# Kernel tuning notes

Hardware: AMD Instinct MI355X
Metric: run time of the kernel (lower is better)

The kernel has to match this reference:

```python
import jax, jax.numpy as jnp
import numpy as np

N = 100000
E = 1600000


def _sage(x, src, dst, wl, wr, b):
    # PyG SAGEConv: out = lin_l(mean_{j in N(i)} x_j) + lin_r(x_i)
    agg = jax.ops.segment_sum(x[src], dst, num_segments=N)
    cnt = jax.ops.segment_sum(jnp.ones((src.shape[0], 1), x.dtype), dst, num_segments=N)
    mean = agg / jnp.maximum(cnt, 1.0)
    return mean @ wl.T + x @ wr.T + b


def _tag(x, src, dst, norm, K, w, b):
    # PyG TAGConv: concat of K+1 hops of D^-1/2 A D^-1/2 propagation, one Linear
    xs = [x]
    h = x
    for _ in range(K):
        h = jax.ops.segment_sum(h[src] * norm[:, None], dst, num_segments=N)
        xs.append(h)
    return jnp.concatenate(xs, axis=1) @ w.T + b


def setup_inputs() -> dict:
    key = jax.random.key(0)
    ks = iter(jax.random.split(key, 32))
    x = jax.random.normal(next(ks), (N, 11), dtype=jnp.float32)
    edge_index = jax.random.randint(next(ks), (2, E), 0, N, dtype=jnp.int64)

    def w(k, o, i):
        return jax.random.normal(k, (o, i), dtype=jnp.float32) / np.sqrt(i)

    p = {
        'sage1_wl': w(next(ks), 128, 11), 'sage1_wr': w(next(ks), 128, 11), 'sage1_b': jnp.zeros((128,), jnp.float32),
        'sage2_wl': w(next(ks), 128, 128), 'sage2_wr': w(next(ks), 128, 128), 'sage2_b': jnp.zeros((128,), jnp.float32),
        'sage3_wl': w(next(ks), 1, 128), 'sage3_wr': w(next(ks), 1, 128), 'sage3_b': jnp.zeros((1,), jnp.float32),
        'tag1a_w': w(next(ks), 8, 44), 'tag1a_b': jnp.zeros((8,), jnp.float32),
        'tag2a_w': w(next(ks), 1, 32), 'tag2a_b': jnp.zeros((1,), jnp.float32),
        'tag1b_w': w(next(ks), 8, 77), 'tag1b_b': jnp.zeros((8,), jnp.float32),
        'tag2b_w': w(next(ks), 1, 56), 'tag2b_b': jnp.zeros((1,), jnp.float32),
        'lin1_w': w(next(ks), 1, 3), 'lin1_b': jnp.zeros((1,), jnp.float32),
    }
    return {'x': x, 'edge_index': edge_index, **p}


def reference(x, edge_index, sage1_wl, sage1_wr, sage1_b, sage2_wl, sage2_wr, sage2_b,
              sage3_wl, sage3_wr, sage3_b, tag1a_w, tag1a_b, tag2a_w, tag2a_b,
              tag1b_w, tag1b_b, tag2b_w, tag2b_b, lin1_w, lin1_b):
    src, dst = edge_index[0], edge_index[1]
    # GCN-style symmetric norm for TAGConv (unit edge weights, no self-loops)
    deg = jax.ops.segment_sum(jnp.ones((E,), x.dtype), dst, num_segments=N)
    dis = jnp.where(deg > 0, deg ** -0.5, 0.0)
    norm = dis[src] * dis[dst]

    x1 = jax.nn.sigmoid(_sage(x, src, dst, sage1_wl, sage1_wr, sage1_b))
    x1 = jax.nn.sigmoid(_sage(x1, src, dst, sage2_wl, sage2_wr, sage2_b))
    x1 = jax.nn.relu(_sage(x1, src, dst, sage3_wl, sage3_wr, sage3_b))

    x2 = jax.nn.sigmoid(_tag(x, src, dst, norm, 3, tag1a_w, tag1a_b))
    x2 = jax.nn.relu(_tag(x2, src, dst, norm, 3, tag2a_w, tag2a_b))

    x3 = jax.nn.sigmoid(_tag(x, src, dst, norm, 6, tag1b_w, tag1b_b))
    x3 = jax.nn.relu(_tag(x3, src, dst, norm, 6, tag2b_w, tag2b_b))

    xc = jnp.concatenate((x1, x2, x3), axis=1)  # [N, 3]
    return jax.nn.relu(xc @ lin1_w.T + lin1_b)  # [N, 1]
```

## Files before the change

kernel.cpp:

```cpp
#include <hip/hip_runtime.h>
#include <hip/hip_bf16.h>
#include <hip/hip_fp16.h>

#define NN 100000
#define EE 1600000
#define NBIN 64
#define BSH 9
#define BSZ 512
#define NBK 196

typedef _Float16 h8v __attribute__((ext_vector_type(8)));
typedef float f4v __attribute__((ext_vector_type(4)));

__device__ __forceinline__ float sigm(float v) { return 1.0f / (1.0f + expf(-v)); }
__device__ __forceinline__ float4 f4add(float4 a, float4 b) {
  a.x += b.x; a.y += b.y; a.z += b.z; a.w += b.w; return a;
}
__device__ __forceinline__ float4 h4f(uint2 v) {
  __half2 a = *reinterpret_cast<__half2*>(&v.x);
  __half2 b = *reinterpret_cast<__half2*>(&v.y);
  float2 fa = __half22float2(a), fb = __half22float2(b);
  return make_float4(fa.x, fa.y, fb.x, fb.y);
}
__device__ __forceinline__ void h8acc(uint4 v, float* a) {
  float4 lo = h4f(make_uint2(v.x, v.y));
  float4 hi = h4f(make_uint2(v.z, v.w));
  a[0] += lo.x; a[1] += lo.y; a[2] += lo.z; a[3] += lo.w;
  a[4] += hi.x; a[5] += hi.y; a[6] += hi.z; a[7] += hi.w;
}
__device__ __forceinline__ uint2 pack4h(float4 r) {
  __half2 q0 = __floats2half2_rn(r.x, r.y), q1 = __floats2half2_rn(r.z, r.w);
  uint2 o; o.x = *(unsigned*)&q0; o.y = *(unsigned*)&q1; return o;
}

#define BH_B 512
#define PREP_B0 ((NN * 12 + 255) / 256)
#define PREP_B1 ((NN + 255) / 256)
__global__ __launch_bounds__(256) void k_bhist_prep(
    const int* __restrict__ ei, int* __restrict__ ghist,
    const float* __restrict__ x, const float* __restrict__ s1wl, const float* __restrict__ s1wr,
    const float* __restrict__ s2wl, const float* __restrict__ s2wr,
    __half* __restrict__ x12h, __half* __restrict__ A32,
    __half* __restrict__ w1h, __half* __restrict__ w2h) {
  __shared__ int lh[NBK];
  int bid = blockIdx.x;
  if (bid < BH_B) {
    for (int j = threadIdx.x; j < NBK; j += 256) lh[j] = 0;
    __syncthreads();
    for (int i = bid * 256 + threadIdx.x; i < EE; i += BH_B * 256)
      atomicAdd(&lh[ei[EE + i] >> BSH], 1);
    __syncthreads();
    for (int j = threadIdx.x; j < NBK; j += 256) {
      int v = lh[j];
      if (v) atomicAdd(&ghist[j], v);
    }
    return;
  }
  int pid = bid - BH_B;
  if (pid < PREP_B0) {
    int i = pid * 256 + threadIdx.x;
    if (i < NN * 12) {
      int n = i / 12, j = i - n * 12;
      x12h[i] = __float2half((j < 11) ? x[n * 11 + j] : 0.0f);
    }
  } else if (pid < PREP_B0 + PREP_B1) {
    int i = (pid - PREP_B0) * 256 + threadIdx.x;
    if (i < NN) {
      float a[11];
      #pragma unroll
      for (int j = 0; j < 11; ++j) a[j] = x[(long)i * 11 + j];
      uint2* row = (uint2*)(A32 + (long)i * 32);
      row[3] = make_uint2(0u, 0u);
      row[4] = pack4h(make_float4(a[0], a[1], a[2], a[3]));
      row[5] = pack4h(make_float4(a[4], a[5], a[6], a[7]));
      row[6] = pack4h(make_float4(a[8], a[9], a[10], 0.0f));
      row[7] = make_uint2(0u, 0u);
    }
  } else if (pid < PREP_B0 + PREP_B1 + 16) {
    int i = (pid - PREP_B0 - PREP_B1) * 256 + threadIdx.x;
    int o = i >> 5, k = i & 31;
    float v = 0.0f;
    if (k < 11) v = s1wl[o * 11 + k];
    else if (k >= 16 && k < 27) v = s1wr[o * 11 + (k - 16)];
    w1h[i] = __float2half(v);
  } else {
    int i = (pid - PREP_B0 - PREP_B1 - 16) * 256 + threadIdx.x;
    int o = i >> 8, k = i & 255;
    float v = (k < 128) ? s2wl[o * 128 + k] : s2wr[o * 128 + (k - 128)];
    w2h[i] = __float2half(v);
  }
}

__global__ void k_b196scan(const int* __restrict__ ghist, int* __restrict__ gcur,
                           int* __restrict__ bexclB, int* __restrict__ csr_off) {
  __shared__ int sh[256];
  int tid = threadIdx.x;
  int v = (tid < NBK) ? ghist[tid] : 0;
  sh[tid] = v;
  __syncthreads();
  for (int d = 1; d < 256; d <<= 1) {
    int t = (tid >= d) ? sh[tid - d] : 0;
    __syncthreads();
    sh[tid] += t;
    __syncthreads();
  }
  int excl = sh[tid] - v;
  if (tid < NBK) { gcur[tid] = excl; bexclB[tid] = excl; }
  if (tid == 0) { bexclB[NBK] = EE; csr_off[NN] = EE; }
}

__global__ __launch_bounds__(256) void k_split(const int* __restrict__ ei,
                                               int* __restrict__ gcur,
                                               unsigned* __restrict__ pairs) {
  __shared__ int cntL[256];
  __shared__ int segO[256];
  __shared__ int curL[256];
  __shared__ int baseL[256];
  __shared__ unsigned stag[4096];
  __shared__ unsigned char bktL[4096];
  int tid = threadIdx.x;
  int tile0 = blockIdx.x * 4096;
  int tcnt = min(4096, EE - tile0);
  cntL[tid] = 0; curL[tid] = 0;
  __syncthreads();
  for (int i = tid; i < tcnt; i += 256)
    atomicAdd(&cntL[ei[EE + tile0 + i] >> BSH], 1);
  __syncthreads();
  int v = cntL[tid];
  segO[tid] = v;
  __syncthreads();
  for (int d = 1; d < 256; d <<= 1) {
    int t = (tid >= d) ? segO[tid - d] : 0;
    __syncthreads();
    segO[tid] += t;
    __syncthreads();
  }
  int excl = segO[tid] - v;
  __syncthreads();
  segO[tid] = excl;
  __syncthreads();
  for (int i = tid; i < tcnt; i += 256) {
    int s = ei[tile0 + i], dd = ei[EE + tile0 + i];
    int b = dd >> BSH;
    int slot = segO[b] + atomicAdd(&curL[b], 1);
    stag[slot] = (unsigned)s | ((unsigned)(dd & (BSZ - 1)) << 17);
    bktL[slot] = (unsigned char)b;
  }
  baseL[tid] = v ? atomicAdd(&gcur[tid], v) : 0;
  __syncthreads();
  for (int i = tid; i < tcnt; i += 256) {
    int b = bktL[i];
    pairs[baseL[b] + (i - segO[b])] = stag[i];
  }
}

__global__ __launch_bounds__(256) void k_bbuild(const unsigned* __restrict__ pairs,
                                                const int* __restrict__ bexclB,
                                                int* __restrict__ cnt, int* __restrict__ csr_off,
                                                float* __restrict__ dis, int* __restrict__ csr_src) {
  __shared__ int c[BSZ];
  __shared__ int ps[256];
  __shared__ int curB[BSZ];
  int tid = threadIdx.x;
  int b = blockIdx.x;
  int lo = b << BSH;
  for (int j = tid; j < BSZ; j += 256) c[j] = 0;
  __syncthreads();
  int s0e = bexclB[b], s1e = bexclB[b + 1];
  for (int i = s0e + tid; i < s1e; i += 256)
    atomicAdd(&c[pairs[i] >> 17], 1);
  __syncthreads();
  int a0 = c[2 * tid], a1 = c[2 * tid + 1];
  int pv = a0 + a1;
  ps[tid] = pv;
  __syncthreads();
  for (int d = 1; d < 256; d <<= 1) {
    int t = (tid >= d) ? ps[tid - d] : 0;
    __syncthreads();
    ps[tid] += t;
    __syncthreads();
  }
  int pex = ps[tid] - pv;
  int base = s0e + pex;
  int n0 = lo + 2 * tid, n1 = n0 + 1;
  if (n0 < NN) {
    csr_off[n0] = base; cnt[n0] = a0;
    dis[n0] = (a0 > 0) ? rsqrtf((float)a0) : 0.0f;
  }
  if (n1 < NN) {
    csr_off[n1] = base + a0; cnt[n1] = a1;
    dis[n1] = (a1 > 0) ? rsqrtf((float)a1) : 0.0f;
  }
  curB[2 * tid] = base;
  curB[2 * tid + 1] = base + a0;
  __syncthreads();
  for (int i = s0e + tid; i < s1e; i += 256) {
    unsigned pk = pairs[i];
    int p = atomicAdd(&curB[pk >> 17], 1);
    csr_src[p] = (int)(pk & 0x1FFFFu);
  }
}

__global__ __launch_bounds__(256) void k_hist(const int* __restrict__ cnt, int* __restrict__ hist) {
  __shared__ int lh[NBIN];
  if (threadIdx.x < NBIN) lh[threadIdx.x] = 0;
  __syncthreads();
  int i = blockIdx.x * 256 + threadIdx.x;
  if (i < NN) atomicAdd(&lh[min(cnt[i], NBIN - 1)], 1);
  __syncthreads();
  if (threadIdx.x < NBIN) {
    int v = lh[threadIdx.x];
    if (v) atomicAdd(&hist[threadIdx.x], v);
  }
}
__global__ void k_binscan(const int* __restrict__ hist, int* __restrict__ bincur) {
  int tid = threadIdx.x;
  int v = hist[tid];
  int incl = v;
  for (int d = 1; d < 64; d <<= 1) {
    int t = __shfl_up(incl, d, 64);
    if (tid >= d) incl += t;
  }
  bincur[tid] = incl - v;
}
__global__ __launch_bounds__(256) void k_scatter(const int* __restrict__ cnt,
                                                 int* __restrict__ bincur,
                                                 int* __restrict__ perm) {
  __shared__ int lh[NBIN];
  __shared__ int lbase[NBIN];
  if (threadIdx.x < NBIN) lh[threadIdx.x] = 0;
  __syncthreads();
  int i = blockIdx.x * 256 + threadIdx.x;
  int b = 0, r = 0;
  bool valid = i < NN;
  if (valid) {
    b = min(cnt[i], NBIN - 1);
    r = atomicAdd(&lh[b], 1);
  }
  __syncthreads();
  if (threadIdx.x < NBIN) {
    int v = lh[threadIdx.x];
    lbase[threadIdx.x] = v ? atomicAdd(&bincur[threadIdx.x], v) : 0;
  }
  __syncthreads();
  if (valid) perm[lbase[b] + r] = i;
}

__global__ void k_gmean12h(const __half* __restrict__ x12h, const int* __restrict__ perm,
                           const int* __restrict__ off, const int* __restrict__ srcarr,
                           __half* __restrict__ A32) {
  int g = blockIdx.x * 64 + (threadIdx.x >> 2);
  int t = threadIdx.x & 3;
  if (g >= NN || t >= 3) return;
  int node = perm[g];
  int s = off[node], e = off[node + 1];
  const uint2* h2 = (const uint2*)x12h;
  float4 acc = {0, 0, 0, 0};
  int p = s;
  for (; p + 4 <= e; p += 4) {
    int s0 = srcarr[p], s1 = srcarr[p + 1], s2 = srcarr[p + 2], s3 = srcarr[p + 3];
    acc = f4add(acc, f4add(f4add(h4f(h2[(long)s0 * 3 + t]), h4f(h2[(long)s1 * 3 + t])),
                           f4add(h4f(h2[(long)s2 * 3 + t]), h4f(h2[(long)s3 * 3 + t]))));
  }
  for (; p < e; ++p) acc = f4add(acc, h4f(h2[(long)srcarr[p] * 3 + t]));
  int c = e - s;
  float inv = 1.0f / (float)(c > 0 ? c : 1);
  acc.x *= inv; acc.y *= inv; acc.z *= inv; acc.w *= inv;
  ((uint2*)A32)[(long)node * 8 + t] = pack4h(acc);
}

__global__ void k_gather128(const __half* __restrict__ h, const int* __restrict__ perm,
                            const int* __restrict__ off, const int* __restrict__ srcarr,
                            __half* __restrict__ outh) {
  int g = blockIdx.x * 16 + (threadIdx.x >> 4);
  int t = threadIdx.x & 15;
  if (g >= NN) return;
  int node = perm[g];
  int s = off[node], e = off[node + 1];
  const uint4* h4 = (const uint4*)h;
  float acc[8] = {};
  int p = s;
  for (; p + 4 <= e; p += 4) {
    int s0 = srcarr[p], s1 = srcarr[p + 1], s2 = srcarr[p + 2], s3 = srcarr[p + 3];
    uint4 r0 = h4[(long)s0 * 16 + t], r1 = h4[(long)s1 * 16 + t];
    uint4 r2 = h4[(long)s2 * 16 + t], r3 = h4[(long)s3 * 16 + t];
    h8acc(r0, acc); h8acc(r1, acc); h8acc(r2, acc); h8acc(r3, acc);
  }
  for (; p < e; ++p) h8acc(h4[(long)srcarr[p] * 16 + t], acc);
  int c = e - s;
  float inv = 1.0f / (float)(c > 0 ? c : 1);
  uint2 lo = pack4h(make_float4(acc[0] * inv, acc[1] * inv, acc[2] * inv, acc[3] * inv));
  uint2 hi = pack4h(make_float4(acc[4] * inv, acc[5] * inv, acc[6] * inv, acc[7] * inv));
  uint4 o; o.x = lo.x; o.y = lo.y; o.z = hi.x; o.w = hi.y;
  ((uint4*)outh)[(long)node * 16 + t] = o;
}

__global__ __launch_bounds__(256) void k_mm1_mfma(
    const __half* __restrict__ A32, const __half* __restrict__ W32,
    const float* __restrict__ bias, __half* __restrict__ out) {
  __shared__ __half lt[4][32][136];
  int tid = threadIdx.x;
  int wave = tid >> 6, l = tid & 63;
  int lr = l & 15, lk = l >> 4;
  int m0 = blockIdx.x * 128 + wave * 32;
  f4v acc[2][8] = {};
  h8v afrag[2];
  #pragma unroll
  for (int rt = 0; rt < 2; ++rt) {
    int row = m0 + rt * 16 + lr;
    h8v z = {};
    afrag[rt] = (row < NN) ? *(const h8v*)&A32[(long)row * 32 + lk * 8] : z;
  }
  #pragma unroll
  for (int c = 0; c < 8; ++c) {
    h8v bfrag = *(const h8v*)&W32[(c * 16 + lr) * 32 + lk * 8];
    acc[0][c] = __builtin_amdgcn_mfma_f32_16x16x32_f16(afrag[0], bfrag, acc[0][c], 0, 0, 0);
    acc[1][c] = __builtin_amdgcn_mfma_f32_16x16x32_f16(afrag[1], bfrag, acc[1][c], 0, 0, 0);
  }
  float bi[8];
  #pragma unroll
  for (int c = 0; c < 8; ++c) bi[c] = bias[c * 16 + lr];
  #pragma unroll
  for (int rt = 0; rt < 2; ++rt)
    #pragma unroll
    for (int c = 0; c < 8; ++c)
      #pragma unroll
      for (int reg = 0; reg < 4; ++reg) {
        float v = acc[rt][c][reg] + bi[c];
        lt[wave][rt * 16 + lk * 4 + reg][c * 16 + lr] = __float2half(sigm(v));
      }
  __syncthreads();
  #pragma unroll
  for (int it = 0; it < 8; ++it) {
    int idx = it * 64 + l;
    int row = idx >> 4, c16 = idx & 15;
    int grow = m0 + row;
    if (grow < NN) {
      uint4 v = *(const uint4*)&lt[wave][row][c16 * 8];
      ((uint4*)out)[(long)grow * 16 + c16] = v;
    }
  }
}

__global__ __launch_bounds__(256) void k_mm2_mfma(
    const __half* __restrict__ A1, const __half* __restrict__ A2,
    const __half* __restrict__ W, const float* __restrict__ bias,
    const float* __restrict__ w3l, const float* __restrict__ w3r,
    float* __restrict__ pp, float* __restrict__ qq) {
  int tid = threadIdx.x;
  int wave = tid >> 6;
  int l = tid & 63;
  int lr = l & 15;
  int lk = l >> 4;
  int m0 = blockIdx.x * 128 + wave * 32;
  f4v acc[2][8] = {};
  #pragma unroll
  for (int ks = 0; ks < 8; ++ks) {
    const __half* Asrc = (ks < 4) ? A1 : A2;
    int kk = (ks & 3) * 32 + lk * 8;
    h8v afrag[2];
    #pragma unroll
    for (int rt = 0; rt < 2; ++rt) {
      int row = m0 + rt * 16 + lr;
      h8v z = {};
      afrag[rt] = (row < NN) ? *(const h8v*)&Asrc[(long)row * 128 + kk] : z;
    }
    #pragma unroll
    for (int c = 0; c < 8; ++c) {
      h8v bfrag = *(const h8v*)&W[(long)(c * 16 + lr) * 256 + ks * 32 + lk * 8];
      acc[0][c] = __builtin_amdgcn_mfma_f32_16x16x32_f16(afrag[0], bfrag, acc[0][c], 0, 0, 0);
      acc[1][c] = __builtin_amdgcn_mfma_f32_16x16x32_f16(afrag[1], bfrag, acc[1][c], 0, 0, 0);
    }
  }
  float wl[8], wr[8], bi[8];
  #pragma unroll
  for (int c = 0; c < 8; ++c) {
    wl[c] = w3l[c * 16 + lr];
    wr[c] = w3r[c * 16 + lr];
    bi[c] = bias[c * 16 + lr];
  }
  #pragma unroll
  for (int rt = 0; rt < 2; ++rt) {
    #pragma unroll
    for (int reg = 0; reg < 4; ++reg) {
      float s1 = 0.0f, s2 = 0.0f;
      #pragma unroll
      for (int c = 0; c < 8; ++c) {
        float v = acc[rt][c][reg] + bi[c];
        float sg = sigm(v);
        s1 += sg * wl[c];
        s2 += sg * wr[c];
      }
      #pragma unroll
      for (int d = 1; d < 16; d <<= 1) {
        s1 += __shfl_xor(s1, d, 64);
        s2 += __shfl_xor(s2, d, 64);
      }
      int row = m0 + rt * 16 + lk * 4 + reg;
      if (lr == 0 && row < NN) { pp[row] = s1; qq[row] = s2; }
    }
  }
}

__global__ __launch_bounds__(256) void k_tag0(
    const float* __restrict__ x, const float* __restrict__ t1aw, const float* __restrict__ t1bw,
    const float* __restrict__ dis,
    float* __restrict__ Pa, float* __restrict__ Pb, __half* __restrict__ PTop,
    const float* __restrict__ pp, const float* __restrict__ qq, const float* __restrict__ s3b,
    const int* __restrict__ perm, const int* __restrict__ csr_off, const int* __restrict__ csr_src,
    float* __restrict__ x1s) {
  for (int i = blockIdx.x * 256 + threadIdx.x; i < NN; i += gridDim.x * 256) {
    float a[11];
    #pragma unroll
    for (int j = 0; j < 11; ++j) a[j] = x[(long)i * 11 + j];
    float dn = dis[i];
    #pragma unroll
    for (int k = 0; k < 4; ++k) {
      float s[8];
      #pragma unroll
      for (int o = 0; o < 8; ++o) {
        float acc = 0.0f;
        #pragma unroll
        for (int j = 0; j < 11; ++j) acc += a[j] * t1aw[o * 44 + k * 11 + j];
        s[o] = acc;
      }
      if (k < 3) {
        float4* dst = (float4*)&Pa[((size_t)k * NN + i) * 8];
        dst[0] = make_float4(s[0], s[1], s[2], s[3]);
        dst[1] = make_float4(s[4], s[5], s[6], s[7]);
      } else {
        uint2 lo = pack4h(make_float4(s[0] * dn, s[1] * dn, s[2] * dn, s[3] * dn));
        uint2 hi = pack4h(make_float4(s[4] * dn, s[5] * dn, s[6] * dn, s[7] * dn));
        uint4 o4; o4.x = lo.x; o4.y = lo.y; o4.z = hi.x; o4.w = hi.y;
        ((uint4*)PTop)[(long)i * 2] = o4;
      }
    }
    #pragma unroll
    for (int k = 0; k < 7; ++k) {
      float s[8];
      #pragma unroll
      for (int o = 0; o < 8; ++o) {
        float acc = 0.0f;
        #pragma unroll
        for (int j = 0; j < 11; ++j) acc += a[j] * t1bw[o * 77 + k * 11 + j];
        s[o] = acc;
      }
      if (k < 6) {
        float4* dst = (float4*)&Pb[((size_t)k * NN + i) * 8];
        dst[0] = make_float4(s[0], s[1], s[2], s[3]);
        dst[1] = make_float4(s[4], s[5], s[6], s[7]);
      } else {
        uint2 lo = pack4h(make_float4(s[0] * dn, s[1] * dn, s[2] * dn, s[3] * dn));
        uint2 hi = pack4h(make_float4(s[4] * dn, s[5] * dn, s[6] * dn, s[7] * dn));
        uint4 o4; o4.x = lo.x; o4.y = lo.y; o4.z = hi.x; o4.w = hi.y;
        ((uint4*)PTop)[(long)i * 2 + 1] = o4;
      }
    }
  }
  int t = threadIdx.x & 3;
  for (int g = blockIdx.x * 64 + (threadIdx.x >> 2); g < NN; g += gridDim.x * 64) {
    int node = perm[g];
    int s = csr_off[node], e = csr_off[node + 1];
    float acc = 0.0f;
    for (int p = s + t; p < e; p += 4) acc += pp[csr_src[p]];
    acc += __shfl_xor(acc, 1, 64); acc += __shfl_xor(acc, 2, 64);
    if (t == 0) {
      int c = e - s;
      float sc = 1.0f / (float)(c > 0 ? c : 1);
      x1s[node] = fmaxf(acc * sc + qq[node] + s3b[0], 0.0f);
    }
  }
}

__global__ __launch_bounds__(256) void k_d8_dual(
    const __half* __restrict__ src, const float* __restrict__ addA,
    const float* __restrict__ addB, __half* __restrict__ dst,
    const int* __restrict__ perm, const int* __restrict__ off,
    const int* __restrict__ srcarr, const float* __restrict__ dis) {
  const uint4* src4 = (const uint4*)src;
  int t = threadIdx.x & 1;
  const float4* addp = (const float4*)(t == 0 ? addA : addB);
  int g = blockIdx.x * 128 + (threadIdx.x >> 1);
  if (g >= NN) return;
  int node = perm[g];
  int s = off[node], e = off[node + 1];
  float acc[8] = {};
  int p = s;
  for (; p + 4 <= e; p += 4) {
    int s0 = srcarr[p], s1 = srcarr[p + 1], s2 = srcarr[p + 2], s3 = srcarr[p + 3];
    h8acc(src4[(long)s0 * 2 + t], acc); h8acc(src4[(long)s1 * 2 + t], acc);
    h8acc(src4[(long)s2 * 2 + t], acc); h8acc(src4[(long)s3 * 2 + t], acc);
  }
  for (; p < e; ++p) h8acc(src4[(long)srcarr[p] * 2 + t], acc);
  float dn = dis[node];
  float4 a0 = addp[(long)node * 2], a1 = addp[(long)node * 2 + 1];
  float4 r0 = make_float4((acc[0] * dn + a0.x) * dn, (acc[1] * dn + a0.y) * dn,
                          (acc[2] * dn + a0.z) * dn, (acc[3] * dn + a0.w) * dn);
  float4 r1 = make_float4((acc[4] * dn + a1.x) * dn, (acc[5] * dn + a1.y) * dn,
                          (acc[6] * dn + a1.z) * dn, (acc[7] * dn + a1.w) * dn);
  uint2 lo = pack4h(r0), hi = pack4h(r1);
  uint4 o; o.x = lo.x; o.y = lo.y; o.z = hi.x; o.w = hi.y;
  ((uint4*)dst)[(long)node * 2 + t] = o;
}

__global__ __launch_bounds__(256) void k_d8_l3(
    const __half* __restrict__ src, const float* __restrict__ Pa0,
    const float* __restrict__ t1ab, const float* __restrict__ t2aw,
    const float* __restrict__ Pb3, __half* __restrict__ dstB, float* __restrict__ P2,
    const int* __restrict__ perm, const int* __restrict__ off,
    const int* __restrict__ srcarr, const float* __restrict__ dis) {
  const uint4* src4 = (const uint4*)src;
  int t = threadIdx.x & 1;
  int g = blockIdx.x * 128 + (threadIdx.x >> 1);
  if (g >= NN) return;
  int node = perm[g];
  int s = off[node], e = off[node + 1];
  float acc[8] = {};
  int p = s;
  for (; p + 4 <= e; p += 4) {
    int s0 = srcarr[p], s1 = srcarr[p + 1], s2 = srcarr[p + 2], s3 = srcarr[p + 3];
    h8acc(src4[(long)s0 * 2 + t], acc); h8acc(src4[(long)s1 * 2 + t], acc);
    h8acc(src4[(long)s2 * 2 + t], acc); h8acc(src4[(long)s3 * 2 + t], acc);
  }
  for (; p < e; ++p) h8acc(src4[(long)srcarr[p] * 2 + t], acc);
  float dn = dis[node];
  if (t == 0) {
    const float4* addp = (const float4*)Pa0;
    float4 a0 = addp[(long)node * 2], a1 = addp[(long)node * 2 + 1];
    float4 b0 = ((const float4*)t1ab)[0], b1 = ((const float4*)t1ab)[1];
    float a[8];
    a[0] = sigm(acc[0] * dn + a0.x + b0.x); a[1] = sigm(acc[1] * dn + a0.y + b0.y);
    a[2] = sigm(acc[2] * dn + a0.z + b0.z); a[3] = sigm(acc[3] * dn + a0.w + b0.w);
    a[4] = sigm(acc[4] * dn + a1.x + b1.x); a[5] = sigm(acc[5] * dn + a1.y + b1.y);
    a[6] = sigm(acc[6] * dn + a1.z + b1.z); a[7] = sigm(acc[7] * dn + a1.w + b1.w);
    #pragma unroll
    for (int k = 0; k < 4; ++k) {
      float sv = 0.0f;
      #pragma unroll
      for (int j = 0; j < 8; ++j) sv += a[j] * t2aw[k * 8 + j];
      if (k == 3) sv *= dn;
      P2[(size_t)k * NN + node] = sv;
    }
  } else {
    const float4* addp = (const float4*)Pb3;
    float4 a0 = addp[(long)node * 2], a1 = addp[(long)node * 2 + 1];
    float4 r0 = make_float4((acc[0] * dn + a0.x) * dn, (acc[1] * dn + a0.y) * dn,
                            (acc[2] * dn + a0.z) * dn, (acc[3] * dn + a0.w) * dn);
    float4 r1 = make_float4((acc[4] * dn + a1.x) * dn, (acc[5] * dn + a1.y) * dn,
                            (acc[6] * dn + a1.z) * dn, (acc[7] * dn + a1.w) * dn);
    uint2 lo = pack4h(r0), hi = pack4h(r1);
    uint4 o; o.x = lo.x; o.y = lo.y; o.z = hi.x; o.w = hi.y;
    ((uint4*)dstB)[(long)node * 2 + 1] = o;
  }
}

__global__ __launch_bounds__(256) void k_d8_single(
    const __half* __restrict__ src, const float* __restrict__ addB, __half* __restrict__ dst,
    const int* __restrict__ perm, const int* __restrict__ off,
    const int* __restrict__ srcarr, const float* __restrict__ dis) {
  const uint2* src2 = (const uint2*)src;
  int t = threadIdx.x & 1;
  int g = blockIdx.x * 128 + (threadIdx.x >> 1);
  if (g >= NN) return;
  int node = perm[g];
  int s = off[node], e = off[node + 1];
  float4 acc = {0, 0, 0, 0};
  int p = s;
  for (; p + 4 <= e; p += 4) {
    int s0 = srcarr[p], s1 = srcarr[p + 1], s2 = srcarr[p + 2], s3 = srcarr[p + 3];
    acc = f4add(acc, f4add(f4add(h4f(src2[(long)s0 * 4 + 2 + t]), h4f(src2[(long)s1 * 4 + 2 + t])),
                           f4add(h4f(src2[(long)s2 * 4 + 2 + t]), h4f(src2[(long)s3 * 4 + 2 + t]))));
  }
  for (; p < e; ++p) acc = f4add(acc, h4f(src2[(long)srcarr[p] * 4 + 2 + t]));
  float dn = dis[node];
  float4 av = ((const float4*)addB)[(long)node * 2 + t];
  float4 r = make_float4((acc.x * dn + av.x) * dn, (acc.y * dn + av.y) * dn,
                         (acc.z * dn + av.z) * dn, (acc.w * dn + av.w) * dn);
  ((uint2*)dst)[(long)node * 4 + 2 + t] = pack4h(r);
}

__global__ __launch_bounds__(256) void k_d8_l6(
    const __half* __restrict__ src, const float* __restrict__ Pb0,
    const float* __restrict__ t1bb, const float* __restrict__ t2bw, float* __restrict__ P2b,
    const int* __restrict__ perm, const int* __restrict__ off,
    const int* __restrict__ srcarr, const float* __restrict__ dis) {
  const uint2* src2 = (const uint2*)src;
  int t = threadIdx.x & 1;
  int g = blockIdx.x * 128 + (threadIdx.x >> 1);
  if (g >= NN) return;
  int node = perm[g];
  int s = off[node], e = off[node + 1];
  float4 acc = {0, 0, 0, 0};
  int p = s;
  for (; p + 4 <= e; p += 4) {
    int s0 = srcarr[p], s1 = srcarr[p + 1], s2 = srcarr[p + 2], s3 = srcarr[p + 3];
    acc = f4add(acc, f4add(f4add(h4f(src2[(long)s0 * 4 + 2 + t]), h4f(src2[(long)s1 * 4 + 2 + t])),
                           f4add(h4f(src2[(long)s2 * 4 + 2 + t]), h4f(src2[(long)s3 * 4 + 2 + t]))));
  }
  for (; p < e; ++p) acc = f4add(acc, h4f(src2[(long)srcarr[p] * 4 + 2 + t]));
  float dn = dis[node];
  float4 av = ((const float4*)Pb0)[(long)node * 2 + t];
  float4 bv = ((const float4*)t1bb)[t];
  float4 r = make_float4(sigm(acc.x * dn + av.x + bv.x), sigm(acc.y * dn + av.y + bv.y),
                         sigm(acc.z * dn + av.z + bv.z), sigm(acc.w * dn + av.w + bv.w));
  float o0 = __shfl_xor(r.x, 1, 64), o1 = __shfl_xor(r.y, 1, 64);
  float o2 = __shfl_xor(r.z, 1, 64), o3 = __shfl_xor(r.w, 1, 64);
  if (t == 0) {
    float a[8] = {r.x, r.y, r.z, r.w, o0, o1, o2, o3};
    #pragma unroll
    for (int k = 0; k < 7; ++k) {
      float sv = 0.0f;
      #pragma unroll
      for (int j = 0; j < 8; ++j) sv += a[j] * t2bw[k * 8 + j];
      if (k == 6) sv *= dn;
      P2b[(size_t)k * NN + node] = sv;
    }
  }
}

template<int MODE>
__global__ void k_g1_dual(
    const float* __restrict__ ua, const float* __restrict__ adda,
    const float* __restrict__ biasa, int acta,
    const float* __restrict__ ub, const float* __restrict__ addb,
    const float* __restrict__ biasb, int actb,
    const int* __restrict__ perm, const int* __restrict__ off,
    const int* __restrict__ srcarr, const float* __restrict__ dis,
    float* __restrict__ outa, float* __restrict__ outb) {
  int g = blockIdx.x * 64 + (threadIdx.x >> 2);
  int t = threadIdx.x & 3;
  if (g >= NN) return;
  int node = perm[g];
  int s = off[node], e = off[node + 1];
  float accA = 0.0f, accB = 0.0f;
  for (int p = s + t; p < e; p += 4) {
    int s0 = srcarr[p];
    accA += ua[s0];
    accB += ub[s0];
  }
  accA += __shfl_xor(accA, 1, 64); accA += __shfl_xor(accA, 2, 64);
  accB += __shfl_xor(accB, 1, 64); accB += __shfl_xor(accB, 2, 64);
  if (t == 0) {
    float sc;
    if (MODE == 0) { int c = e - s; sc = 1.0f / (float)(c > 0 ? c : 1); }
    else sc = dis[node];
    float rA = accA * sc + adda[node];
    if (biasa) rA += biasa[0];
    if (acta == 3) rA *= sc; else if (acta == 2) rA = fmaxf(rA, 0.0f);
    outa[node] = rA;
    float rB = accB * sc + addb[node];
    if (biasb) rB += biasb[0];
    if (actb == 3) rB *= sc; else if (actb == 2) rB = fmaxf(rB, 0.0f);
    outb[node] = rB;
  }
}

template<int MODE>
__global__ void k_g1_single(
    const float* __restrict__ ua, const float* __restrict__ adda,
    const float* __restrict__ biasa, int acta,
    const int* __restrict__ perm, const int* __restrict__ off,
    const int* __restrict__ srcarr, const float* __restrict__ dis,
    float* __restrict__ outa) {
  int g = blockIdx.x * 64 + (threadIdx.x >> 2);
  int t = threadIdx.x & 3;
  if (g >= NN) return;
  int node = perm[g];
  int s = off[node], e = off[node + 1];
  float accA = 0.0f;
  for (int p = s + t; p < e; p += 4) accA += ua[srcarr[p]];
  accA += __shfl_xor(accA, 1, 64); accA += __shfl_xor(accA, 2, 64);
  if (t == 0) {
    float sc;
    if (MODE == 0) { int c = e - s; sc = 1.0f / (float)(c > 0 ? c : 1); }
    else sc = dis[node];
    float rA = accA * sc + adda[node];
    if (biasa) rA += biasa[0];
    if (acta == 3) rA *= sc; else if (acta == 2) rA = fmaxf(rA, 0.0f);
    outa[node] = rA;
  }
}

__global__ void k_g1_final(
    const float* __restrict__ ua, const float* __restrict__ adda,
    const float* __restrict__ biasa,
    const float* __restrict__ x1s, const float* __restrict__ x2s,
    const float* __restrict__ lw, const float* __restrict__ lb,
    const int* __restrict__ perm, const int* __restrict__ off,
    const int* __restrict__ srcarr, const float* __restrict__ dis,
    float* __restrict__ out) {
  int g = blockIdx.x * 64 + (threadIdx.x >> 2);
  int t = threadIdx.x & 3;
  if (g >= NN) return;
  int node = perm[g];
  int s = off[node], e = off[node + 1];
  float accA = 0.0f;
  for (int p = s + t; p < e; p += 4) accA += ua[srcarr[p]];
  accA += __shfl_xor(accA, 1, 64); accA += __shfl_xor(accA, 2, 64);
  if (t == 0) {
    float x3v = fmaxf(accA * dis[node] + adda[node] + biasa[0], 0.0f);
    float v = x1s[node] * lw[0] + x2s[node] * lw[1] + x3v * lw[2] + lb[0];
    out[node] = fmaxf(v, 0.0f);
  }
}

extern "C" void kernel_launch(void* const* d_in, const int* in_sizes, int n_in,
                              void* d_out, int out_size, void* d_ws, size_t ws_size,
                              hipStream_t stream) {
  const float* x    = (const float*)d_in[0];
  const int*   ei   = (const int*)d_in[1];
  const float* s1wl = (const float*)d_in[2];
  const float* s1wr = (const float*)d_in[3];
  const float* s1b  = (const float*)d_in[4];
  const float* s2wl = (const float*)d_in[5];
  const float* s2wr = (const float*)d_in[6];
  const float* s2b  = (const float*)d_in[7];
  const float* s3wl = (const float*)d_in[8];
  const float* s3wr = (const float*)d_in[9];
  const float* s3b  = (const float*)d_in[10];
  const float* t1aw = (const float*)d_in[11];
  const float* t1ab = (const float*)d_in[12];
  const float* t2aw = (const float*)d_in[13];
  const float* t2ab = (const float*)d_in[14];
  const float* t1bw = (const float*)d_in[15];
  const float* t1bb = (const float*)d_in[16];
  const float* t2bw = (const float*)d_in[17];
  const float* t2bb = (const float*)d_in[18];
  const float* lw   = (const float*)d_in[19];
  const float* lb   = (const float*)d_in[20];
  float* out = (float*)d_out;

  char* basep = (char*)d_ws;
  size_t off = 0;
  auto alloc = [&](size_t bytes) -> void* {
    void* ptr = basep + off;
    off = (off + bytes + 255) & ~(size_t)255;
    return ptr;
  };
  int*      cnt     = (int*)alloc((size_t)NN * 4);
  int*      csr_off = (int*)alloc((size_t)(NN + 1) * 4);
  float*    dis     = (float*)alloc((size_t)NN * 4);
  int*      csr_src = (int*)alloc((size_t)EE * 4);
  unsigned* pairs   = (unsigned*)alloc((size_t)EE * 4);
  int*      perm    = (int*)alloc((size_t)NN * 4);
  int*      ghist   = (int*)alloc(256 * 4);
  int*      gcur    = (int*)alloc(256 * 4);
  int*      bexclB  = (int*)alloc(256 * 4);
  int*      hist    = (int*)alloc(NBIN * 4);
  int*      bincur  = (int*)alloc(NBIN * 4);
  float*    x1s     = (float*)alloc((size_t)NN * 4);
  float*    x2s     = (float*)alloc((size_t)NN * 4);
  float*    pp      = (float*)alloc((size_t)NN * 4);
  float*    qq      = (float*)alloc((size_t)NN * 4);
  float*    uA1     = (float*)alloc((size_t)NN * 4);
  float*    uA2     = (float*)alloc((size_t)NN * 4);
  float*    uB1     = (float*)alloc((size_t)NN * 4);
  float*    uB2     = (float*)alloc((size_t)NN * 4);
  __half*   x12h    = (__half*)alloc((size_t)NN * 12 * 2);
  __half*   A32     = (__half*)alloc((size_t)NN * 32 * 2);
  __half*   w1h     = (__half*)alloc((size_t)128 * 32 * 2);
  __half*   w2h     = (__half*)alloc((size_t)128 * 256 * 2);
  __half*   x1a_h   = (__half*)alloc((size_t)NN * 128 * 2);
  __half*   mean128_h = (__half*)alloc((size_t)NN * 128 * 2);
  float*    region2 = (float*)alloc((size_t)NN * 56 * 4);

  float* r1 = (float*)x1a_h;
  float*  Pa    = r1;
  __half* PTop  = (__half*)(r1 + (size_t)NN * 24);
  __half* zbuf0 = (__half*)(r1 + (size_t)NN * 32);
  __half* zbuf1 = (__half*)(r1 + (size_t)NN * 40);
  float*  P2    = r1 + (size_t)NN * 48;
  float*  Pb    = region2;
  float*  P2b   = region2 + (size_t)NN * 48;

  const size_t S8 = (size_t)NN * 8;
  const size_t S1 = (size_t)NN;

  hipMemsetAsync(ghist, 0, 3840, stream);
  k_bhist_prep<<<BH_B + PREP_B0 + PREP_B1 + 16 + 128, 256, 0, stream>>>(
      ei, ghist, x, s1wl, s1wr, s2wl, s2wr, x12h, A32, w1h, w2h);
  k_b196scan<<<1, 256, 0, stream>>>(ghist, gcur, bexclB, csr_off);
  k_split<<<(EE + 4095) / 4096, 256, 0, stream>>>(ei, gcur, pairs);
  k_bbuild<<<NBK, 256, 0, stream>>>(pairs, bexclB, cnt, csr_off, dis, csr_src);

  k_hist<<<(NN + 255) / 256, 256, 0, stream>>>(cnt, hist);
  k_binscan<<<1, 64, 0, stream>>>(hist, bincur);
  k_scatter<<<(NN + 255) / 256, 256, 0, stream>>>(cnt, bincur, perm);

  k_gmean12h<<<(NN + 63) / 64, 256, 0, stream>>>(x12h, perm, csr_off, csr_src, A32);
  k_mm1_mfma<<<(NN + 127) / 128, 256, 0, stream>>>(A32, w1h, s1b, x1a_h);
  k_gather128<<<(NN + 15) / 16, 256, 0, stream>>>(x1a_h, perm, csr_off, csr_src, mean128_h);
  k_mm2_mfma<<<(NN + 127) / 128, 256, 0, stream>>>(mean128_h, x1a_h, w2h, s2b, s3wl, s3wr, pp, qq);

  k_tag0<<<(NN + 63) / 64, 256, 0, stream>>>(
      x, t1aw, t1bw, dis, Pa, Pb, PTop, pp, qq, s3b, perm, csr_off, csr_src, x1s);
  k_d8_dual<<<(NN + 127) / 128, 256, 0, stream>>>(
      PTop, Pa + 2 * S8, Pb + 5 * S8, zbuf0, perm, csr_off, csr_src, dis);
  k_d8_dual<<<(NN + 127) / 128, 256, 0, stream>>>(
      zbuf0, Pa + 1 * S8, Pb + 4 * S8, zbuf1, perm, csr_off, csr_src, dis);
  k_d8_l3<<<(NN + 127) / 128, 256, 0, stream>>>(
      zbuf1, Pa, t1ab, t2aw, Pb + 3 * S8, zbuf0, P2, perm, csr_off, csr_src, dis);
  k_d8_single<<<(NN + 127) / 128, 256, 0, stream>>>(
      zbuf0, Pb + 2 * S8, zbuf1, perm, csr_off, csr_src, dis);
  k_d8_single<<<(NN + 127) / 128, 256, 0, stream>>>(
      zbuf1, Pb + 1 * S8, zbuf0, perm, csr_off, csr_src, dis);
  k_d8_l6<<<(NN + 127) / 128, 256, 0, stream>>>(
      zbuf0, Pb, t1bb, t2bw, P2b, perm, csr_off, csr_src, dis);

  k_g1_dual<1><<<(NN + 63) / 64, 256, 0, stream>>>(
      P2 + 3 * S1, P2 + 2 * S1, nullptr, 3,
      P2b + 6 * S1, P2b + 5 * S1, nullptr, 3,
      perm, csr_off, csr_src, dis, uA1, uB1);
  k_g1_dual<1><<<(NN + 63) / 64, 256, 0, stream>>>(
      uA1, P2 + 1 * S1, nullptr, 3,
      uB1, P2b + 4 * S1, nullptr, 3,
      perm, csr_off, csr_src, dis, uA2, uB2);
  k_g1_dual<1><<<(NN + 63) / 64, 256, 0, stream>>>(
      uA2, P2, t2ab, 2,
      uB2, P2b + 3 * S1, nullptr, 3,
      perm, csr_off, csr_src, dis, x2s, uB1);
  k_g1_single<1><<<(NN + 63) / 64, 256, 0, stream>>>(
      uB1, P2b + 2 * S1, nullptr, 3, perm, csr_off, csr_src, dis, uB2);
  k_g1_single<1><<<(NN + 63) / 64, 256, 0, stream>>>(
      uB2, P2b + 1 * S1, nullptr, 3, perm, csr_off, csr_src, dis, uB1);
  k_g1_final<<<(NN + 63) / 64, 256, 0, stream>>>(
      uB1, P2b, t2bb, x1s, x2s, lw, lb, perm, csr_off, csr_src, dis, out);
}
```

Baseline: 509.0 us.

## Co-schedule independent SAGE and TAG stages in horizontally fused kernels

Independent stages of the SAGE chain and the TAG hop chains are merged into shared launches. A block-index range selects which body each block runs, so the branches can execute concurrently and fewer serial launches are needed. The degree histogram is also folded into the CSR build kernel, which removes a separate pass over the counts. Intermediate buffers that used to alias the SAGE activations now get their own allocations so the overlapping stages do not clobber each other. The cost is more device memory and larger kernels whose block types use different amounts of registers and shared memory, which may lower occupancy.

```diff
diff --git a/kernel.cpp b/kernel.cpp
--- a/kernel.cpp
+++ b/kernel.cpp
@@ -8,6 +8,12 @@
 #define BSH 9
 #define BSZ 512
 #define NBK 196
+
+#define GA 1563
+#define GT 391
+#define GM 782
+#define GG 6250
+#define G1 1563
 
 typedef _Float16 h8v __attribute__((ext_vector_type(8)));
 typedef float f4v __attribute__((ext_vector_type(4)));
@@ -157,14 +163,17 @@
 __global__ __launch_bounds__(256) void k_bbuild(const unsigned* __restrict__ pairs,
                                                 const int* __restrict__ bexclB,
                                                 int* __restrict__ cnt, int* __restrict__ csr_off,
-                                                float* __restrict__ dis, int* __restrict__ csr_src) {
+                                                float* __restrict__ dis, int* __restrict__ csr_src,
+                                                int* __restrict__ hist) {
   __shared__ int c[BSZ];
   __shared__ int ps[256];
   __shared__ int curB[BSZ];
+  __shared__ int lhist[NBIN];
   int tid = threadIdx.x;
   int b = blockIdx.x;
   int lo = b << BSH;
   for (int j = tid; j < BSZ; j += 256) c[j] = 0;
+  if (tid < NBIN) lhist[tid] = 0;
   __syncthreads();
   int s0e = bexclB[b], s1e = bexclB[b + 1];
   for (int i = s0e + tid; i < s1e; i += 256)
@@ -186,10 +195,12 @@
   if (n0 < NN) {
     csr_off[n0] = base; cnt[n0] = a0;
     dis[n0] = (a0 > 0) ? rsqrtf((float)a0) : 0.0f;
+    atomicAdd(&lhist[min(a0, NBIN - 1)], 1);
   }
   if (n1 < NN) {
     csr_off[n1] = base + a0; cnt[n1] = a1;
     dis[n1] = (a1 > 0) ? rsqrtf((float)a1) : 0.0f;
+    atomicAdd(&lhist[min(a1, NBIN - 1)], 1);
   }
   curB[2 * tid] = base;
   curB[2 * tid + 1] = base + a0;
@@ -199,20 +210,13 @@
     int p = atomicAdd(&curB[pk >> 17], 1);
     csr_src[p] = (int)(pk & 0x1FFFFu);
   }
-}
-
-__global__ __launch_bounds__(256) void k_hist(const int* __restrict__ cnt, int* __restrict__ hist) {
-  __shared__ int lh[NBIN];
-  if (threadIdx.x < NBIN) lh[threadIdx.x] = 0;
-  __syncthreads();
-  int i = blockIdx.x * 256 + threadIdx.x;
-  if (i < NN) atomicAdd(&lh[min(cnt[i], NBIN - 1)], 1);
-  __syncthreads();
-  if (threadIdx.x < NBIN) {
-    int v = lh[threadIdx.x];
-    if (v) atomicAdd(&hist[threadIdx.x], v);
-  }
-}
+  __syncthreads();
+  if (tid < NBIN) {
+    int v = lhist[tid];
+    if (v) atomicAdd(&hist[tid], v);
+  }
+}
+
 __global__ void k_binscan(const int* __restrict__ hist, int* __restrict__ bincur) {
   int tid = threadIdx.x;
   int v = hist[tid];
@@ -246,10 +250,9 @@
   if (valid) perm[lbase[b] + r] = i;
 }
 
-__global__ void k_gmean12h(const __half* __restrict__ x12h, const int* __restrict__ perm,
-                           const int* __restrict__ off, const int* __restrict__ srcarr,
-                           __half* __restrict__ A32) {
-  int g = blockIdx.x * 64 + (threadIdx.x >> 2);
+__device__ void gmean12h_body(int bid, const __half* x12h, const int* perm,
+                              const int* off, const int* srcarr, __half* A32) {
+  int g = bid * 64 + (threadIdx.x >> 2);
   int t = threadIdx.x & 3;
   if (g >= NN || t >= 3) return;
   int node = perm[g];
@@ -269,10 +272,241 @@
   ((uint2*)A32)[(long)node * 8 + t] = pack4h(acc);
 }
 
-__global__ void k_gather128(const __half* __restrict__ h, const int* __restrict__ perm,
-                            const int* __restrict__ off, const int* __restrict__ srcarr,
-                            __half* __restrict__ outh) {
-  int g = blockIdx.x * 16 + (threadIdx.x >> 4);
+__device__ void tagp8_body(int bid, const float* x, const float* t1aw, const float* t1bw,
+                           const float* dis, float* Pa, float* Pb, __half* PTop) {
+  int i = bid * 256 + threadIdx.x;
+  if (i >= NN) return;
+  float a[11];
+  #pragma unroll
+  for (int j = 0; j < 11; ++j) a[j] = x[(long)i * 11 + j];
+  float dn = dis[i];
+  #pragma unroll
+  for (int k = 0; k < 4; ++k) {
+    float s[8];
+    #pragma unroll
+    for (int o = 0; o < 8; ++o) {
+      float acc = 0.0f;
+      #pragma unroll
+      for (int j = 0; j < 11; ++j) acc += a[j] * t1aw[o * 44 + k * 11 + j];
+      s[o] = acc;
+    }
+    if (k < 3) {
+      float4* dst = (float4*)&Pa[((size_t)k * NN + i) * 8];
+      dst[0] = make_float4(s[0], s[1], s[2], s[3]);
+      dst[1] = make_float4(s[4], s[5], s[6], s[7]);
+    } else {
+      uint2 lo = pack4h(make_float4(s[0] * dn, s[1] * dn, s[2] * dn, s[3] * dn));
+      uint2 hi = pack4h(make_float4(s[4] * dn, s[5] * dn, s[6] * dn, s[7] * dn));
+      uint4 o4; o4.x = lo.x; o4.y = lo.y; o4.z = hi.x; o4.w = hi.y;
+      ((uint4*)PTop)[(long)i * 2] = o4;
+    }
+  }
+  #pragma unroll
+  for (int k = 0; k < 7; ++k) {
+    float s[8];
+    #pragma unroll
+    for (int o = 0; o < 8; ++o) {
+      float acc = 0.0f;
+      #pragma unroll
+      for (int j = 0; j < 11; ++j) acc += a[j] * t1bw[o * 77 + k * 11 + j];
+      s[o] = acc;
+    }
+    if (k < 6) {
+      float4* dst = (float4*)&Pb[((size_t)k * NN + i) * 8];
+      dst[0] = make_float4(s[0], s[1], s[2], s[3]);
+      dst[1] = make_float4(s[4], s[5], s[6], s[7]);
+    } else {
+      uint2 lo = pack4h(make_float4(s[0] * dn, s[1] * dn, s[2] * dn, s[3] * dn));
+      uint2 hi = pack4h(make_float4(s[4] * dn, s[5] * dn, s[6] * dn, s[7] * dn));
+      uint4 o4; o4.x = lo.x; o4.y = lo.y; o4.z = hi.x; o4.w = hi.y;
+      ((uint4*)PTop)[(long)i * 2 + 1] = o4;
+    }
+  }
+}
+
+__device__ void d8_dual_body(int bid, const __half* src, const float* addA,
+                             const float* addB, __half* dst,
+                             const int* perm, const int* off,
+                             const int* srcarr, const float* dis) {
+  const uint4* src4 = (const uint4*)src;
+  int t = threadIdx.x & 1;
+  const float4* addp = (const float4*)(t == 0 ? addA : addB);
+  int g = bid * 128 + (threadIdx.x >> 1);
+  if (g >= NN) return;
+  int node = perm[g];
+  int s = off[node], e = off[node + 1];
+  float acc[8] = {};
+  int p = s;
+  for (; p + 4 <= e; p += 4) {
+    int s0 = srcarr[p], s1 = srcarr[p + 1], s2 = srcarr[p + 2], s3 = srcarr[p + 3];
+    h8acc(src4[(long)s0 * 2 + t], acc); h8acc(src4[(long)s1 * 2 + t], acc);
+    h8acc(src4[(long)s2 * 2 + t], acc); h8acc(src4[(long)s3 * 2 + t], acc);
+  }
+  for (; p < e; ++p) h8acc(src4[(long)srcarr[p] * 2 + t], acc);
+  float dn = dis[node];
+  float4 a0 = addp[(long)node * 2], a1 = addp[(long)node * 2 + 1];
+  float4 r0 = make_float4((acc[0] * dn + a0.x) * dn, (acc[1] * dn + a0.y) * dn,
+                          (acc[2] * dn + a0.z) * dn, (acc[3] * dn + a0.w) * dn);
+  float4 r1 = make_float4((acc[4] * dn + a1.x) * dn, (acc[5] * dn + a1.y) * dn,
+                          (acc[6] * dn + a1.z) * dn, (acc[7] * dn + a1.w) * dn);
+  uint2 lo = pack4h(r0), hi = pack4h(r1);
+  uint4 o; o.x = lo.x; o.y = lo.y; o.z = hi.x; o.w = hi.y;
+  ((uint4*)dst)[(long)node * 2 + t] = o;
+}
+
+__device__ void d8_l3_body(int bid, const __half* src, const float* Pa0,
+                           const float* t1ab, const float* t2aw,
+                           const float* Pb3, __half* dstB, float* P2,
+                           const int* perm, const int* off,
+                           const int* srcarr, const float* dis) {
+  const uint4* src4 = (const uint4*)src;
+  int t = threadIdx.x & 1;
+  int g = bid * 128 + (threadIdx.x >> 1);
+  if (g >= NN) return;
+  int node = perm[g];
+  int s = off[node], e = off[node + 1];
+  float acc[8] = {};
+  int p = s;
+  for (; p + 4 <= e; p += 4) {
+    int s0 = srcarr[p], s1 = srcarr[p + 1], s2 = srcarr[p + 2], s3 = srcarr[p + 3];
+    h8acc(src4[(long)s0 * 2 + t], acc); h8acc(src4[(long)s1 * 2 + t], acc);
+    h8acc(src4[(long)s2 * 2 + t], acc); h8acc(src4[(long)s3 * 2 + t], acc);
+  }
+  for (; p < e; ++p) h8acc(src4[(long)srcarr[p] * 2 + t], acc);
+  float dn = dis[node];
+  if (t == 0) {
+    const float4* addp = (const float4*)Pa0;
+    float4 a0 = addp[(long)node * 2], a1 = addp[(long)node * 2 + 1];
+    float4 b0 = ((const float4*)t1ab)[0], b1 = ((const float4*)t1ab)[1];
+    float a[8];
+    a[0] = sigm(acc[0] * dn + a0.x + b0.x); a[1] = sigm(acc[1] * dn + a0.y + b0.y);
+    a[2] = sigm(acc[2] * dn + a0.z + b0.z); a[3] = sigm(acc[3] * dn + a0.w + b0.w);
+    a[4] = sigm(acc[4] * dn + a1.x + b1.x); a[5] = sigm(acc[5] * dn + a1.y + b1.y);
+    a[6] = sigm(acc[6] * dn + a1.z + b1.z); a[7] = sigm(acc[7] * dn + a1.w + b1.w);
+    #pragma unroll
+    for (int k = 0; k < 4; ++k) {
+      float sv = 0.0f;
+      #pragma unroll
+      for (int j = 0; j < 8; ++j) sv += a[j] * t2aw[k * 8 + j];
+      if (k == 3) sv *= dn;
+      P2[(size_t)k * NN + node] = sv;
+    }
+  } else {
+    const float4* addp = (const float4*)Pb3;
+    float4 a0 = addp[(long)node * 2], a1 = addp[(long)node * 2 + 1];
+    float4 r0 = make_float4((acc[0] * dn + a0.x) * dn, (acc[1] * dn + a0.y) * dn,
+                            (acc[2] * dn + a0.z) * dn, (acc[3] * dn + a0.w) * dn);
+    float4 r1 = make_float4((acc[4] * dn + a1.x) * dn, (acc[5] * dn + a1.y) * dn,
+                            (acc[6] * dn + a1.z) * dn, (acc[7] * dn + a1.w) * dn);
+    uint2 lo = pack4h(r0), hi = pack4h(r1);
+    uint4 o; o.x = lo.x; o.y = lo.y; o.z = hi.x; o.w = hi.y;
+    ((uint4*)dstB)[(long)node * 2 + 1] = o;
+  }
+}
+
+__device__ void d8_single_body(int bid, const __half* src, const float* addB, __half* dst,
+                               const int* perm, const int* off,
+                               const int* srcarr, const float* dis) {
+  const uint2* src2 = (const uint2*)src;
+  int t = threadIdx.x & 1;
+  int g = bid * 128 + (threadIdx.x >> 1);
+  if (g >= NN) return;
+  int node = perm[g];
+  int s = off[node], e = off[node + 1];
+  float4 acc = {0, 0, 0, 0};
+  int p = s;
+  for (; p + 4 <= e; p += 4) {
+    int s0 = srcarr[p], s1 = srcarr[p + 1], s2 = srcarr[p + 2], s3 = srcarr[p + 3];
+    acc = f4add(acc, f4add(f4add(h4f(src2[(long)s0 * 4 + 2 + t]), h4f(src2[(long)s1 * 4 + 2 + t])),
+                           f4add(h4f(src2[(long)s2 * 4 + 2 + t]), h4f(src2[(long)s3 * 4 + 2 + t]))));
+  }
+  for (; p < e; ++p) acc = f4add(acc, h4f(src2[(long)srcarr[p] * 4 + 2 + t]));
+  float dn = dis[node];
+  float4 av = ((const float4*)addB)[(long)node * 2 + t];
+  float4 r = make_float4((acc.x * dn + av.x) * dn, (acc.y * dn + av.y) * dn,
+                         (acc.z * dn + av.z) * dn, (acc.w * dn + av.w) * dn);
+  ((uint2*)dst)[(long)node * 4 + 2 + t] = pack4h(r);
+}
+
+__device__ void d8_l6_body(int bid, const __half* src, const float* Pb0,
+                           const float* t1bb, const float* t2bw, float* P2b,
+                           const int* perm, const int* off,
+                           const int* srcarr, const float* dis) {
+  const uint2* src2 = (const uint2*)src;
+  int t = threadIdx.x & 1;
+  int g = bid * 128 + (threadIdx.x >> 1);
+  if (g >= NN) return;
+  int node = perm[g];
+  int s = off[node], e = off[node + 1];
+  float4 acc = {0, 0, 0, 0};
+  int p = s;
+  for (; p + 4 <= e; p += 4) {
+    int s0 = srcarr[p], s1 = srcarr[p + 1], s2 = srcarr[p + 2], s3 = srcarr[p + 3];
+    acc = f4add(acc, f4add(f4add(h4f(src2[(long)s0 * 4 + 2 + t]), h4f(src2[(long)s1 * 4 + 2 + t])),
+                           f4add(h4f(src2[(long)s2 * 4 + 2 + t]), h4f(src2[(long)s3 * 4 + 2 + t]))));
+  }
+  for (; p < e; ++p) acc = f4add(acc, h4f(src2[(long)srcarr[p] * 4 + 2 + t]));
+  float dn = dis[node];
+  float4 av = ((const float4*)Pb0)[(long)node * 2 + t];
+  float4 bv = ((const float4*)t1bb)[t];
+  float4 r = make_float4(sigm(acc.x * dn + av.x + bv.x), sigm(acc.y * dn + av.y + bv.y),
+                         sigm(acc.z * dn + av.z + bv.z), sigm(acc.w * dn + av.w + bv.w));
+  float o0 = __shfl_xor(r.x, 1, 64), o1 = __shfl_xor(r.y, 1, 64);
+  float o2 = __shfl_xor(r.z, 1, 64), o3 = __shfl_xor(r.w, 1, 64);
+  if (t == 0) {
+    float a[8] = {r.x, r.y, r.z, r.w, o0, o1, o2, o3};
+    #pragma unroll
+    for (int k = 0; k < 7; ++k) {
+      float sv = 0.0f;
+      #pragma unroll
+      for (int j = 0; j < 8; ++j) sv += a[j] * t2bw[k * 8 + j];
+      if (k == 6) sv *= dn;
+      P2b[(size_t)k * NN + node] = sv;
+    }
+  }
+}
+
+__device__ void d1_body(int bid, const float* ua, const float* adda, const float* bias,
+                        int act, float* outa, const int* perm, const int* off,
+                        const int* srcarr, const float* dis) {
+  int g = bid * 64 + (threadIdx.x >> 2);
+  int t = threadIdx.x & 3;
+  if (g >= NN) return;
+  int node = perm[g];
+  int s = off[node], e = off[node + 1];
+  float accA = 0.0f;
+  for (int p = s + t; p < e; p += 4) accA += ua[srcarr[p]];
+  accA += __shfl_xor(accA, 1, 64); accA += __shfl_xor(accA, 2, 64);
+  if (t == 0) {
+    float sc = dis[node];
+    float rA = accA * sc + adda[node];
+    if (bias) rA += bias[0];
+    if (act == 3) rA *= sc; else if (act == 2) rA = fmaxf(rA, 0.0f);
+    outa[node] = rA;
+  }
+}
+
+__device__ void x1s_body(int bid, const float* pp, const float* qq, const float* s3b,
+                         const int* perm, const int* off, const int* srcarr,
+                         float* x1s) {
+  int g = bid * 64 + (threadIdx.x >> 2);
+  int t = threadIdx.x & 3;
+  if (g >= NN) return;
+  int node = perm[g];
+  int s = off[node], e = off[node + 1];
+  float acc = 0.0f;
+  for (int p = s + t; p < e; p += 4) acc += pp[srcarr[p]];
+  acc += __shfl_xor(acc, 1, 64); acc += __shfl_xor(acc, 2, 64);
+  if (t == 0) {
+    int c = e - s;
+    float sc = 1.0f / (float)(c > 0 ? c : 1);
+    x1s[node] = fmaxf(acc * sc + qq[node] + s3b[0], 0.0f);
+  }
+}
+
+__device__ void gather128_body(int bid, const __half* h, const int* perm,
+                               const int* off, const int* srcarr, __half* outh) {
+  int g = bid * 16 + (threadIdx.x >> 4);
   int t = threadIdx.x & 15;
   if (g >= NN) return;
   int node = perm[g];
@@ -295,14 +529,12 @@
   ((uint4*)outh)[(long)node * 16 + t] = o;
 }
 
-__global__ __launch_bounds__(256) void k_mm1_mfma(
-    const __half* __restrict__ A32, const __half* __restrict__ W32,
-    const float* __restrict__ bias, __half* __restrict__ out) {
-  __shared__ __half lt[4][32][136];
+__device__ void mm1_body(int bid, const __half* A32, const __half* W32,
+                         const float* bias, __half* out, __half (*lt)[32][136]) {
   int tid = threadIdx.x;
   int wave = tid >> 6, l = tid & 63;
   int lr = l & 15, lk = l >> 4;
-  int m0 = blockIdx.x * 128 + wave * 32;
+  int m0 = bid * 128 + wave * 32;
   f4v acc[2][8] = {};
   h8v afrag[2];
   #pragma unroll
@@ -342,17 +574,16 @@
   }
 }
 
-__global__ __launch_bounds__(256) void k_mm2_mfma(
-    const __half* __restrict__ A1, const __half* __restrict__ A2,
-    const __half* __restrict__ W, const float* __restrict__ bias,
-    const float* __restrict__ w3l, const float* __restrict__ w3r,
-    float* __restrict__ pp, float* __restrict__ qq) {
+__device__ void mm2_body(int bid, const __half* A1, const __half* A2,
+                         const __half* W, const float* bias,
+                         const float* w3l, const float* w3r,
+                         float* pp, float* qq) {
   int tid = threadIdx.x;
   int wave = tid >> 6;
   int l = tid & 63;
   int lr = l & 15;
   int lk = l >> 4;
-  int m0 = blockIdx.x * 128 + wave * 32;
+  int m0 = bid * 128 + wave * 32;
   f4v acc[2][8] = {};
   #pragma unroll
   for (int ks = 0; ks < 8; ++ks) {
@@ -402,293 +633,89 @@
   }
 }
 
-__global__ __launch_bounds__(256) void k_tag0(
-    const float* __restrict__ x, const float* __restrict__ t1aw, const float* __restrict__ t1bw,
-    const float* __restrict__ dis,
-    float* __restrict__ Pa, float* __restrict__ Pb, __half* __restrict__ PTop,
-    const float* __restrict__ pp, const float* __restrict__ qq, const float* __restrict__ s3b,
-    const int* __restrict__ perm, const int* __restrict__ csr_off, const int* __restrict__ csr_src,
-    float* __restrict__ x1s) {
-  for (int i = blockIdx.x * 256 + threadIdx.x; i < NN; i += gridDim.x * 256) {
-    float a[11];
-    #pragma unroll
-    for (int j = 0; j < 11; ++j) a[j] = x[(long)i * 11 + j];
-    float dn = dis[i];
-    #pragma unroll
-    for (int k = 0; k < 4; ++k) {
-      float s[8];
-      #pragma unroll
-      for (int o = 0; o < 8; ++o) {
-        float acc = 0.0f;
-        #pragma unroll
-        for (int j = 0; j < 11; ++j) acc += a[j] * t1aw[o * 44 + k * 11 + j];
-        s[o] = acc;
-      }
-      if (k < 3) {
-        float4* dst = (float4*)&Pa[((size_t)k * NN + i) * 8];
-        dst[0] = make_float4(s[0], s[1], s[2], s[3]);
-        dst[1] = make_float4(s[4], s[5], s[6], s[7]);
-      } else {
-        uint2 lo = pack4h(make_float4(s[0] * dn, s[1] * dn, s[2] * dn, s[3] * dn));
-        uint2 hi = pack4h(make_float4(s[4] * dn, s[5] * dn, s[6] * dn, s[7] * dn));
-        uint4 o4; o4.x = lo.x; o4.y = lo.y; o4.z = hi.x; o4.w = hi.y;
-        ((uint4*)PTop)[(long)i * 2] = o4;
-      }
-    }
-    #pragma unroll
-    for (int k = 0; k < 7; ++k) {
-      float s[8];
-      #pragma unroll
-      for (int o = 0; o < 8; ++o) {
-        float acc = 0.0f;
-        #pragma unroll
-        for (int j = 0; j < 11; ++j) acc += a[j] * t1bw[o * 77 + k * 11 + j];
-        s[o] = acc;
-      }
-      if (k < 6) {
-        float4* dst = (float4*)&Pb[((size_t)k * NN + i) * 8];
-        dst[0] = make_float4(s[0], s[1], s[2], s[3]);
-        dst[1] = make_float4(s[4], s[5], s[6], s[7]);
-      } else {
-        uint2 lo = pack4h(make_float4(s[0] * dn, s[1] * dn, s[2] * dn, s[3] * dn));
-        uint2 hi = pack4h(make_float4(s[4] * dn, s[5] * dn, s[6] * dn, s[7] * dn));
-        uint4 o4; o4.x = lo.x; o4.y = lo.y; o4.z = hi.x; o4.w = hi.y;
-        ((uint4*)PTop)[(long)i * 2 + 1] = o4;
-      }
-    }
-  }
-  int t = threadIdx.x & 3;
-  for (int g = blockIdx.x * 64 + (threadIdx.x >> 2); g < NN; g += gridDim.x * 64) {
-    int node = perm[g];
-    int s = csr_off[node], e = csr_off[node + 1];
-    float acc = 0.0f;
-    for (int p = s + t; p < e; p += 4) acc += pp[csr_src[p]];
-    acc += __shfl_xor(acc, 1, 64); acc += __shfl_xor(acc, 2, 64);
-    if (t == 0) {
-      int c = e - s;
-      float sc = 1.0f / (float)(c > 0 ? c : 1);
-      x1s[node] = fmaxf(acc * sc + qq[node] + s3b[0], 0.0f);
-    }
-  }
-}
-
-__global__ __launch_bounds__(256) void k_d8_dual(
-    const __half* __restrict__ src, const float* __restrict__ addA,
-    const float* __restrict__ addB, __half* __restrict__ dst,
-    const int* __restrict__ perm, const int* __restrict__ off,
-    const int* __restrict__ srcarr, const float* __restrict__ dis) {
-  const uint4* src4 = (const uint4*)src;
-  int t = threadIdx.x & 1;
-  const float4* addp = (const float4*)(t == 0 ? addA : addB);
-  int g = blockIdx.x * 128 + (threadIdx.x >> 1);
-  if (g >= NN) return;
-  int node = perm[g];
-  int s = off[node], e = off[node + 1];
-  float acc[8] = {};
-  int p = s;
-  for (; p + 4 <= e; p += 4) {
-    int s0 = srcarr[p], s1 = srcarr[p + 1], s2 = srcarr[p + 2], s3 = srcarr[p + 3];
-    h8acc(src4[(long)s0 * 2 + t], acc); h8acc(src4[(long)s1 * 2 + t], acc);
-    h8acc(src4[(long)s2 * 2 + t], acc); h8acc(src4[(long)s3 * 2 + t], acc);
-  }
-  for (; p < e; ++p) h8acc(src4[(long)srcarr[p] * 2 + t], acc);
-  float dn = dis[node];
-  float4 a0 = addp[(long)node * 2], a1 = addp[(long)node * 2 + 1];
-  float4 r0 = make_float4((acc[0] * dn + a0.x) * dn, (acc[1] * dn + a0.y) * dn,
-                          (acc[2] * dn + a0.z) * dn, (acc[3] * dn + a0.w) * dn);
-  float4 r1 = make_float4((acc[4] * dn + a1.x) * dn, (acc[5] * dn + a1.y) * dn,
-                          (acc[6] * dn + a1.z) * dn, (acc[7] * dn + a1.w) * dn);
-  uint2 lo = pack4h(r0), hi = pack4h(r1);
-  uint4 o; o.x = lo.x; o.y = lo.y; o.z = hi.x; o.w = hi.y;
-  ((uint4*)dst)[(long)node * 2 + t] = o;
-}
-
-__global__ __launch_bounds__(256) void k_d8_l3(
-    const __half* __restrict__ src, const float* __restrict__ Pa0,
-    const float* __restrict__ t1ab, const float* __restrict__ t2aw,
-    const float* __restrict__ Pb3, __half* __restrict__ dstB, float* __restrict__ P2,
-    const int* __restrict__ perm, const int* __restrict__ off,
-    const int* __restrict__ srcarr, const float* __restrict__ dis) {
-  const uint4* src4 = (const uint4*)src;
-  int t = threadIdx.x & 1;
-  int g = blockIdx.x * 128 + (threadIdx.x >> 1);
-  if (g >= NN) return;
-  int node = perm[g];
-  int s = off[node], e = off[node + 1];
-  float acc[8] = {};
-  int p = s;
-  for (; p + 4 <= e; p += 4) {
-    int s0 = srcarr[p], s1 = srcarr[p + 1], s2 = srcarr[p + 2], s3 = srcarr[p + 3];
-    h8acc(src4[(long)s0 * 2 + t], acc); h8acc(src4[(long)s1 * 2 + t], acc);
-    h8acc(src4[(long)s2 * 2 + t], acc); h8acc(src4[(long)s3 * 2 + t], acc);
-  }
-  for (; p < e; ++p) h8acc(src4[(long)srcarr[p] * 2 + t], acc);
-  float dn = dis[node];
-  if (t == 0) {
-    const float4* addp = (const float4*)Pa0;
-    float4 a0 = addp[(long)node * 2], a1 = addp[(long)node * 2 + 1];
-    float4 b0 = ((const float4*)t1ab)[0], b1 = ((const float4*)t1ab)[1];
-    float a[8];
-    a[0] = sigm(acc[0] * dn + a0.x + b0.x); a[1] = sigm(acc[1] * dn + a0.y + b0.y);
-    a[2] = sigm(acc[2] * dn + a0.z + b0.z); a[3] = sigm(acc[3] * dn + a0.w + b0.w);
-    a[4] = sigm(acc[4] * dn + a1.x + b1.x); a[5] = sigm(acc[5] * dn + a1.y + b1.y);
-    a[6] = sigm(acc[6] * dn + a1.z + b1.z); a[7] = sigm(acc[7] * dn + a1.w + b1.w);
-    #pragma unroll
-    for (int k = 0; k < 4; ++k) {
-      float sv = 0.0f;
-      #pragma unroll
-      for (int j = 0; j < 8; ++j) sv += a[j] * t2aw[k * 8 + j];
-      if (k == 3) sv *= dn;
-      P2[(size_t)k * NN + node] = sv;
-    }
-  } else {
-    const float4* addp = (const float4*)Pb3;
-    float4 a0 = addp[(long)node * 2], a1 = addp[(long)node * 2 + 1];
-    float4 r0 = make_float4((acc[0] * dn + a0.x) * dn, (acc[1] * dn + a0.y) * dn,
-                            (acc[2] * dn + a0.z) * dn, (acc[3] * dn + a0.w) * dn);
-    float4 r1 = make_float4((acc[4] * dn + a1.x) * dn, (acc[5] * dn + a1.y) * dn,
-                            (acc[6] * dn + a1.z) * dn, (acc[7] * dn + a1.w) * dn);
-    uint2 lo = pack4h(r0), hi = pack4h(r1);
-    uint4 o; o.x = lo.x; o.y = lo.y; o.z = hi.x; o.w = hi.y;
-    ((uint4*)dstB)[(long)node * 2 + 1] = o;
-  }
-}
-
-__global__ __launch_bounds__(256) void k_d8_single(
-    const __half* __restrict__ src, const float* __restrict__ addB, __half* __restrict__ dst,
-    const int* __restrict__ perm, const int* __restrict__ off,
-    const int* __restrict__ srcarr, const float* __restrict__ dis) {
-  const uint2* src2 = (const uint2*)src;
-  int t = threadIdx.x & 1;
-  int g = blockIdx.x * 128 + (threadIdx.x >> 1);
-  if (g >= NN) return;
-  int node = perm[g];
-  int s = off[node], e = off[node + 1];
-  float4 acc = {0, 0, 0, 0};
-  int p = s;
-  for (; p + 4 <= e; p += 4) {
-    int s0 = srcarr[p], s1 = srcarr[p + 1], s2 = srcarr[p + 2], s3 = srcarr[p + 3];
-    acc = f4add(acc, f4add(f4add(h4f(src2[(long)s0 * 4 + 2 + t]), h4f(src2[(long)s1 * 4 + 2 + t])),
-                           f4add(h4f(src2[(long)s2 * 4 + 2 + t]), h4f(src2[(long)s3 * 4 + 2 + t]))));
-  }
-  for (; p < e; ++p) acc = f4add(acc, h4f(src2[(long)srcarr[p] * 4 + 2 + t]));
-  float dn = dis[node];
-  float4 av = ((const float4*)addB)[(long)node * 2 + t];
-  float4 r = make_float4((acc.x * dn + av.x) * dn, (acc.y * dn + av.y) * dn,
-                         (acc.z * dn + av.z) * dn, (acc.w * dn + av.w) * dn);
-  ((uint2*)dst)[(long)node * 4 + 2 + t] = pack4h(r);
-}
-
-__global__ __launch_bounds__(256) void k_d8_l6(
-    const __half* __restrict__ src, const float* __restrict__ Pb0,
-    const float* __restrict__ t1bb, const float* __restrict__ t2bw, float* __restrict__ P2b,
-    const int* __restrict__ perm, const int* __restrict__ off,
-    const int* __restrict__ srcarr, const float* __restrict__ dis) {
-  const uint2* src2 = (const uint2*)src;
-  int t = threadIdx.x & 1;
-  int g = blockIdx.x * 128 + (threadIdx.x >> 1);
-  if (g >= NN) return;
-  int node = perm[g];
-  int s = off[node], e = off[node + 1];
-  float4 acc = {0, 0, 0, 0};
-  int p = s;
-  for (; p + 4 <= e; p += 4) {
-    int s0 = srcarr[p], s1 = srcarr[p + 1], s2 = srcarr[p + 2], s3 = srcarr[p + 3];
-    acc = f4add(acc, f4add(f4add(h4f(src2[(long)s0 * 4 + 2 + t]), h4f(src2[(long)s1 * 4 + 2 + t])),
-                           f4add(h4f(src2[(long)s2 * 4 + 2 + t]), h4f(src2[(long)s3 * 4 + 2 + t]))));
-  }
-  for (; p < e; ++p) acc = f4add(acc, h4f(src2[(long)srcarr[p] * 4 + 2 + t]));
-  float dn = dis[node];
-  float4 av = ((const float4*)Pb0)[(long)node * 2 + t];
-  float4 bv = ((const float4*)t1bb)[t];
-  float4 r = make_float4(sigm(acc.x * dn + av.x + bv.x), sigm(acc.y * dn + av.y + bv.y),
-                         sigm(acc.z * dn + av.z + bv.z), sigm(acc.w * dn + av.w + bv.w));
-  float o0 = __shfl_xor(r.x, 1, 64), o1 = __shfl_xor(r.y, 1, 64);
-  float o2 = __shfl_xor(r.z, 1, 64), o3 = __shfl_xor(r.w, 1, 64);
-  if (t == 0) {
-    float a[8] = {r.x, r.y, r.z, r.w, o0, o1, o2, o3};
-    #pragma unroll
-    for (int k = 0; k < 7; ++k) {
-      float sv = 0.0f;
-      #pragma unroll
-      for (int j = 0; j < 8; ++j) sv += a[j] * t2bw[k * 8 + j];
-      if (k == 6) sv *= dn;
-      P2b[(size_t)k * NN + node] = sv;
-    }
-  }
-}
-
-template<int MODE>
-__global__ void k_g1_dual(
-    const float* __restrict__ ua, const float* __restrict__ adda,
-    const float* __restrict__ biasa, int acta,
-    const float* __restrict__ ub, const float* __restrict__ addb,
-    const float* __restrict__ biasb, int actb,
-    const int* __restrict__ perm, const int* __restrict__ off,
-    const int* __restrict__ srcarr, const float* __restrict__ dis,
-    float* __restrict__ outa, float* __restrict__ outb) {
-  int g = blockIdx.x * 64 + (threadIdx.x >> 2);
-  int t = threadIdx.x & 3;
-  if (g >= NN) return;
-  int node = perm[g];
-  int s = off[node], e = off[node + 1];
-  float accA = 0.0f, accB = 0.0f;
-  for (int p = s + t; p < e; p += 4) {
-    int s0 = srcarr[p];
-    accA += ua[s0];
-    accB += ub[s0];
-  }
-  accA += __shfl_xor(accA, 1, 64); accA += __shfl_xor(accA, 2, 64);
-  accB += __shfl_xor(accB, 1, 64); accB += __shfl_xor(accB, 2, 64);
-  if (t == 0) {
-    float sc;
-    if (MODE == 0) { int c = e - s; sc = 1.0f / (float)(c > 0 ? c : 1); }
-    else sc = dis[node];
-    float rA = accA * sc + adda[node];
-    if (biasa) rA += biasa[0];
-    if (acta == 3) rA *= sc; else if (acta == 2) rA = fmaxf(rA, 0.0f);
-    outa[node] = rA;
-    float rB = accB * sc + addb[node];
-    if (biasb) rB += biasb[0];
-    if (actb == 3) rB *= sc; else if (actb == 2) rB = fmaxf(rB, 0.0f);
-    outb[node] = rB;
-  }
-}
-
-template<int MODE>
-__global__ void k_g1_single(
-    const float* __restrict__ ua, const float* __restrict__ adda,
-    const float* __restrict__ biasa, int acta,
-    const int* __restrict__ perm, const int* __restrict__ off,
-    const int* __restrict__ srcarr, const float* __restrict__ dis,
-    float* __restrict__ outa) {
-  int g = blockIdx.x * 64 + (threadIdx.x >> 2);
-  int t = threadIdx.x & 3;
-  if (g >= NN) return;
-  int node = perm[g];
-  int s = off[node], e = off[node + 1];
-  float accA = 0.0f;
-  for (int p = s + t; p < e; p += 4) accA += ua[srcarr[p]];
-  accA += __shfl_xor(accA, 1, 64); accA += __shfl_xor(accA, 2, 64);
-  if (t == 0) {
-    float sc;
-    if (MODE == 0) { int c = e - s; sc = 1.0f / (float)(c > 0 ? c : 1); }
-    else sc = dis[node];
-    float rA = accA * sc + adda[node];
-    if (biasa) rA += biasa[0];
-    if (acta == 3) rA *= sc; else if (acta == 2) rA = fmaxf(rA, 0.0f);
-    outa[node] = rA;
-  }
-}
-
-__global__ void k_g1_final(
-    const float* __restrict__ ua, const float* __restrict__ adda,
-    const float* __restrict__ biasa,
-    const float* __restrict__ x1s, const float* __restrict__ x2s,
-    const float* __restrict__ lw, const float* __restrict__ lb,
-    const int* __restrict__ perm, const int* __restrict__ off,
-    const int* __restrict__ srcarr, const float* __restrict__ dis,
-    float* __restrict__ out) {
+__global__ __launch_bounds__(256) void k_fuseA(
+    const __half* x12h, const int* perm, const int* off, const int* srcarr, __half* A32,
+    const float* x, const float* t1aw, const float* t1bw, const float* dis,
+    float* Pa, float* Pb, __half* PTop) {
+  if (blockIdx.x < GA) gmean12h_body(blockIdx.x, x12h, perm, off, srcarr, A32);
+  else tagp8_body(blockIdx.x - GA, x, t1aw, t1bw, dis, Pa, Pb, PTop);
+}
+
+__global__ __launch_bounds__(256) void k_fuseB(
+    const __half* A32, const __half* W32, const float* s1b, __half* x1a,
+    const __half* PTop, const float* Pa2, const float* Pb5, __half* zbuf0,
+    const int* perm, const int* off, const int* srcarr, const float* dis) {
+  __shared__ __half lt[4][32][136];
+  if (blockIdx.x < GM) mm1_body(blockIdx.x, A32, W32, s1b, x1a, lt);
+  else d8_dual_body(blockIdx.x - GM, PTop, Pa2, Pb5, zbuf0, perm, off, srcarr, dis);
+}
+
+__global__ __launch_bounds__(256) void k_fuseC(
+    const __half* x1a, __half* mean128,
+    const __half* zbuf0, const float* Pa1, const float* Pb4, __half* zbuf1,
+    const int* perm, const int* off, const int* srcarr, const float* dis) {
+  if (blockIdx.x < GG) gather128_body(blockIdx.x, x1a, perm, off, srcarr, mean128);
+  else d8_dual_body(blockIdx.x - GG, zbuf0, Pa1, Pb4, zbuf1, perm, off, srcarr, dis);
+}
+
+__global__ __launch_bounds__(256) void k_fuseD(
+    const __half* mean128, const __half* x1a, const __half* w2h, const float* s2b,
+    const float* w3l, const float* w3r, float* pp, float* qq,
+    const __half* zbuf1, const float* Pa0, const float* t1ab, const float* t2aw,
+    const float* Pb3, __half* zbuf0, float* P2,
+    const int* perm, const int* off, const int* srcarr, const float* dis) {
+  if (blockIdx.x < GM) mm2_body(blockIdx.x, mean128, x1a, w2h, s2b, w3l, w3r, pp, qq);
+  else d8_l3_body(blockIdx.x - GM, zbuf1, Pa0, t1ab, t2aw, Pb3, zbuf0, P2,
+                  perm, off, srcarr, dis);
+}
+
+__global__ __launch_bounds__(256) void k_fuseE(
+    const __half* zbuf0, const float* Pb2, __half* zbuf1,
+    const float* pp, const float* qq, const float* s3b, float* x1s,
+    const float* P2, float* uA1,
+    const int* perm, const int* off, const int* srcarr, const float* dis) {
+  if (blockIdx.x < GM)
+    d8_single_body(blockIdx.x, zbuf0, Pb2, zbuf1, perm, off, srcarr, dis);
+  else if (blockIdx.x < GM + G1)
+    x1s_body(blockIdx.x - GM, pp, qq, s3b, perm, off, srcarr, x1s);
+  else
+    d1_body(blockIdx.x - GM - G1, P2 + 3 * (size_t)NN, P2 + 2 * (size_t)NN,
+            nullptr, 3, uA1, perm, off, srcarr, dis);
+}
+
+__global__ __launch_bounds__(256) void k_fuseF(
+    const __half* zbuf1, const float* Pb1, __half* zbuf0,
+    const float* uA1, const float* P2, float* uA2,
+    const int* perm, const int* off, const int* srcarr, const float* dis) {
+  if (blockIdx.x < GM)
+    d8_single_body(blockIdx.x, zbuf1, Pb1, zbuf0, perm, off, srcarr, dis);
+  else
+    d1_body(blockIdx.x - GM, uA1, P2 + 1 * (size_t)NN, nullptr, 3, uA2,
+            perm, off, srcarr, dis);
+}
+
+__global__ __launch_bounds__(256) void k_fuseG(
+    const __half* zbuf0, const float* Pb0, const float* t1bb, const float* t2bw,
+    float* P2b, const float* uA2, const float* P2, const float* t2ab, float* x2s,
+    const int* perm, const int* off, const int* srcarr, const float* dis) {
+  if (blockIdx.x < GM)
+    d8_l6_body(blockIdx.x, zbuf0, Pb0, t1bb, t2bw, P2b, perm, off, srcarr, dis);
+  else
+    d1_body(blockIdx.x - GM, uA2, P2, t2ab, 2, x2s, perm, off, srcarr, dis);
+}
+
+__global__ __launch_bounds__(256) void k_d1b(
+    const float* ua, const float* adda, float* outa,
+    const int* perm, const int* off, const int* srcarr, const float* dis) {
+  d1_body(blockIdx.x, ua, adda, nullptr, 3, outa, perm, off, srcarr, dis);
+}
+
+__global__ __launch_bounds__(256) void k_g1_final(
+    const float* ua, const float* adda, const float* biasa,
+    const float* x1s, const float* x2s,
+    const float* lw, const float* lb,
+    const int* perm, const int* off, const int* srcarr, const float* dis,
+    float* out) {
   int g = blockIdx.x * 64 + (threadIdx.x >> 2);
   int t = threadIdx.x & 3;
   if (g >= NN) return;
@@ -762,16 +789,13 @@
   __half*   w2h     = (__half*)alloc((size_t)128 * 256 * 2);
   __half*   x1a_h   = (__half*)alloc((size_t)NN * 128 * 2);
   __half*   mean128_h = (__half*)alloc((size_t)NN * 128 * 2);
-  float*    region2 = (float*)alloc((size_t)NN * 56 * 4);
-
-  float* r1 = (float*)x1a_h;
-  float*  Pa    = r1;
-  __half* PTop  = (__half*)(r1 + (size_t)NN * 24);
-  __half* zbuf0 = (__half*)(r1 + (size_t)NN * 32);
-  __half* zbuf1 = (__half*)(r1 + (size_t)NN * 40);
-  float*  P2    = r1 + (size_t)NN * 48;
-  float*  Pb    = region2;
-  float*  P2b   = region2 + (size_t)NN * 48;
+  float*    Pa    = (float*)alloc((size_t)NN * 24 * 4);
+  float*    Pb    = (float*)alloc((size_t)NN * 48 * 4);
+  __half*   PTop  = (__half*)alloc((size_t)NN * 16 * 2);
+  __half*   zbuf0 = (__half*)alloc((size_t)NN * 16 * 2);
+  __half*   zbuf1 = (__half*)alloc((size_t)NN * 16 * 2);
+  float*    P2    = (float*)alloc((size_t)NN * 4 * 4);
+  float*    P2b   = (float*)alloc((size_t)NN * 7 * 4);
 
   const size_t S8 = (size_t)NN * 8;
   const size_t S1 = (size_t)NN;
@@ -781,48 +805,37 @@
       ei, ghist, x, s1wl, s1wr, s2wl, s2wr, x12h, A32, w1h, w2h);
   k_b196scan<<<1, 256, 0, stream>>>(ghist, gcur, bexclB, csr_off);
   k_split<<<(EE + 4095) / 4096, 256, 0, stream>>>(ei, gcur, pairs);
-  k_bbuild<<<NBK, 256, 0, stream>>>(pairs, bexclB, cnt, csr_off, dis, csr_src);
-
-  k_hist<<<(NN + 255) / 256, 256, 0, stream>>>(cnt, hist);
+  k_bbuild<<<NBK, 256, 0, stream>>>(pairs, bexclB, cnt, csr_off, dis, csr_src, hist);
   k_binscan<<<1, 64, 0, stream>>>(hist, bincur);
   k_scatter<<<(NN + 255) / 256, 256, 0, stream>>>(cnt, bincur, perm);
 
-  k_gmean12h<<<(NN + 63) / 64, 256, 0, stream>>>(x12h, perm, csr_off, csr_src, A32);
-  k_mm1_mfma<<<(NN + 127) / 128, 256, 0, stream>>>(A32, w1h, s1b, x1a_h);
-  k_gather128<<<(NN + 15) / 16, 256, 0, stream>>>(x1a_h, perm, csr_off, csr_src, mean128_h);
-  k_mm2_mfma<<<(NN + 127) / 128, 256, 0, stream>>>(mean128_h, x1a_h, w2h, s2b, s3wl, s3wr, pp, qq);
-
-  k_tag0<<<(NN + 63) / 64, 256, 0, stream>>>(
-      x, t1aw, t1bw, dis, Pa, Pb, PTop, pp, qq, s3b, perm, csr_off, csr_src, x1s);
-  k_d8_dual<<<(NN + 127) / 128, 256, 0, stream>>>(
-      PTop, Pa + 2 * S8, Pb + 5 * S8, zbuf0, perm, csr_off, csr_src, dis);
-  k_d8_dual<<<(NN + 127) / 128, 256, 0, stream>>>(
-      zbuf0, Pa + 1 * S8, Pb + 4 * S8, zbuf1, perm, csr_off, csr_src, dis);
-  k_d8_l3<<<(NN + 127) / 128, 256, 0, stream>>>(
-      zbuf1, Pa, t1ab, t2aw, Pb + 3 * S8, zbuf0, P2, perm, csr_off, csr_src, dis);
-  k_d8_single<<<(NN + 127) / 128, 256, 0, stream>>>(
-      zbuf0, Pb + 2 * S8, zbuf1, perm, csr_off, csr_src, dis);
-  k_d8_single<<<(NN + 127) / 128, 256, 0, stream>>>(
-      zbuf1, Pb + 1 * S8, zbuf0, perm, csr_off, csr_src, dis);
-  k_d8_l6<<<(NN + 127) / 128, 256, 0, stream>>>(
-      zbuf0, Pb, t1bb, t2bw, P2b, perm, csr_off, csr_src, dis);
-
-  k_g1_dual<1><<<(NN + 63) / 64, 256, 0, stream>>>(
-      P2 + 3 * S1, P2 + 2 * S1, nullptr, 3,
-      P2b + 6 * S1, P2b + 5 * S1, nullptr, 3,
-      perm, csr_off, csr_src, dis, uA1, uB1);
-  k_g1_dual<1><<<(NN + 63) / 64, 256, 0, stream>>>(
-      uA1, P2 + 1 * S1, nullptr, 3,
-      uB1, P2b + 4 * S1, nullptr, 3,
-      perm, csr_off, csr_src, dis, uA2, uB2);
-  k_g1_dual<1><<<(NN + 63) / 64, 256, 0, stream>>>(
-      uA2, P2, t2ab, 2,
-      uB2, P2b + 3 * S1, nullptr, 3,
-      perm, csr_off, csr_src, dis, x2s, uB1);
-  k_g1_single<1><<<(NN + 63) / 64, 256, 0, stream>>>(
-      uB1, P2b + 2 * S1, nullptr, 3, perm, csr_off, csr_src, dis, uB2);
-  k_g1_single<1><<<(NN + 63) / 64, 256, 0, stream>>>(
-      uB2, P2b + 1 * S1, nullptr, 3, perm, csr_off, csr_src, dis, uB1);
-  k_g1_final<<<(NN + 63) / 64, 256, 0, stream>>>(
+  k_fuseA<<<GA + GT, 256, 0, stream>>>(
+      x12h, perm, csr_off, csr_src, A32, x, t1aw, t1bw, dis, Pa, Pb, PTop);
+  k_fuseB<<<GM + GM, 256, 0, stream>>>(
+      A32, w1h, s1b, x1a_h, PTop, Pa + 2 * S8, Pb + 5 * S8, zbuf0,
+      perm, csr_off, csr_src, dis);
+  k_fuseC<<<GG + GM, 256, 0, stream>>>(
+      x1a_h, mean128_h, zbuf0, Pa + 1 * S8, Pb + 4 * S8, zbuf1,
+      perm, csr_off, csr_src, dis);
+  k_fuseD<<<GM + GM, 256, 0, stream>>>(
+      mean128_h, x1a_h, w2h, s2b, s3wl, s3wr, pp, qq,
+      zbuf1, Pa, t1ab, t2aw, Pb + 3 * S8, zbuf0, P2,
+      perm, csr_off, csr_src, dis);
+  k_fuseE<<<GM + G1 + G1, 256, 0, stream>>>(
+      zbuf0, Pb + 2 * S8, zbuf1, pp, qq, s3b, x1s, P2, uA1,
+      perm, csr_off, csr_src, dis);
+  k_fuseF<<<GM + G1, 256, 0, stream>>>(
+      zbuf1, Pb + 1 * S8, zbuf0, uA1, P2, uA2,
+      perm, csr_off, csr_src, dis);
+  k_fuseG<<<GM + G1, 256, 0, stream>>>(
+      zbuf0, Pb, t1bb, t2bw, P2b, uA2, P2, t2ab, x2s,
+      perm, csr_off, csr_src, dis);
+
+  k_d1b<<<G1, 256, 0, stream>>>(P2b + 6 * S1, P2b + 5 * S1, uB1, perm, csr_off, csr_src, dis);
+  k_d1b<<<G1, 256, 0, stream>>>(uB1, P2b + 4 * S1, uB2, perm, csr_off, csr_src, dis);
+  k_d1b<<<G1, 256, 0, stream>>>(uB2, P2b + 3 * S1, uB1, perm, csr_off, csr_src, dis);
+  k_d1b<<<G1, 256, 0, stream>>>(uB1, P2b + 2 * S1, uB2, perm, csr_off, csr_src, dis);
+  k_d1b<<<G1, 256, 0, stream>>>(uB2, P2b + 1 * S1, uB1, perm, csr_off, csr_src, dis);
+  k_g1_final<<<G1, 256, 0, stream>>>(
       uB1, P2b, t2bb, x1s, x2s, lw, lb, perm, csr_off, csr_src, dis, out);
 }
```

New measurement: 487.7 us. -4.2%, faster.
